# Kernel tuning notes

Measured on AMD Instinct MI355X. Metric: run time of the kernel, lower is better.

## Reference

```python
import jax, jax.numpy as jnp
import numpy as np

B, N, D_M, H, D_K, R, GRID = 2, 2048, 128, 8, 16, 4, 64


def setup_inputs() -> dict:
    key = jax.random.key(0)
    ks = jax.random.split(key, 12)
    z = jax.random.normal(ks[0], (B, N, D_M), dtype=jnp.float32)
    patch_token = jax.random.normal(ks[1], (B, 1, D_M), dtype=jnp.float32)
    positions = jax.random.randint(ks[2], (B, N, 2), 0, GRID, dtype=jnp.int32)
    alive_mask = (jax.random.uniform(ks[3], (B, N, 1)) > 0.1).astype(jnp.float32)
    s = 0.02
    Wq = jax.random.normal(ks[4], (D_M, H * D_K), dtype=jnp.float32) * s
    Wk = jax.random.normal(ks[5], (D_M, H * D_K), dtype=jnp.float32) * s
    Wv = jax.random.normal(ks[6], (D_M, H * D_K), dtype=jnp.float32) * s
    Wo = jax.random.normal(ks[7], (H * D_K, D_M), dtype=jnp.float32) * s
    bq = jnp.zeros((H * D_K,), jnp.float32)
    bk = jnp.zeros((H * D_K,), jnp.float32)
    bv = jnp.zeros((H * D_K,), jnp.float32)
    bo = jnp.zeros((D_M,), jnp.float32)
    rel_bias = jax.random.normal(ks[8], (H, 2 * R + 1, 2 * R + 1), dtype=jnp.float32) * s
    return {"z": z, "patch_token": patch_token, "positions": positions, "alive_mask": alive_mask,
            "Wq": Wq, "bq": bq, "Wk": Wk, "bk": bk, "Wv": Wv, "bv": bv, "Wo": Wo, "bo": bo,
            "rel_bias": rel_bias}


def reference(z, patch_token, positions, alive_mask, Wq, bq, Wk, bk, Wv, bv, Wo, bo, rel_bias):
    B_, N_, _ = z.shape
    H_ = rel_bias.shape[0]
    R_ = (rel_bias.shape[1] - 1) // 2
    dk = Wq.shape[1] // H_
    alive = alive_mask                                   # [B,N,1] float 0/1
    z_a = z * alive
    tokens = jnp.concatenate([z_a, patch_token], axis=1)  # [B,N+1,d_m]
    q = (z_a @ Wq + bq).reshape(B_, N_, H_, dk).transpose(0, 2, 1, 3)       # [B,H,N,dk]
    k = (tokens @ Wk + bk).reshape(B_, N_ + 1, H_, dk).transpose(0, 2, 1, 3)
    v = (tokens @ Wv + bv).reshape(B_, N_ + 1, H_, dk).transpose(0, 2, 1, 3)
    q = q * alive[:, None]                               # [B,1,N,1] broadcast
    logits = jnp.einsum('bhnd,bhmd->bhnm', q, k) / jnp.sqrt(jnp.float32(dk))  # [B,H,N,N+1]
    # Chebyshev mask (delta = pos_i - pos_j)
    delta = positions[:, :, None, :] - positions[:, None, :, :]               # [B,N,N,2]
    cheb = jnp.maximum(jnp.abs(delta[..., 0]), jnp.abs(delta[..., 1]))
    alive_j = alive[:, :, 0] > 0
    not_self = ~jnp.eye(N_, dtype=bool)
    allowed = (cheb <= R_) & alive_j[:, None, :] & not_self[None]
    mask_agents = jnp.where(allowed, 0.0, -1e9).astype(jnp.float32)           # [B,N,N]
    # Relative-position bias (torch uses delta_rel = pos_j - pos_i = -delta)
    dx = -delta[..., 0] + R_
    dy = -delta[..., 1] + R_
    valid = (dx >= 0) & (dx <= 2 * R_) & (dy >= 0) & (dy <= 2 * R_)
    flat = jnp.clip(dx, 0, 2 * R_) * (2 * R_ + 1) + jnp.clip(dy, 0, 2 * R_)   # [B,N,N] int
    table = rel_bias.reshape(H_, -1)
    rel = jnp.moveaxis(jnp.take(table, flat, axis=1), 0, 1)                   # [B,H,N,N]
    rel = rel * valid[:, None].astype(jnp.float32)
    add = mask_agents[:, None] + rel                                          # [B,H,N,N]
    logits = logits + jnp.pad(add, ((0, 0), (0, 0), (0, 0), (0, 1)))          # patch col: mask 0, no bias
    logits = jnp.where(alive[:, None] > 0, logits, -1e9)                      # dead queries
    attn = jax.nn.softmax(logits, axis=-1)
    out = jnp.einsum('bhnm,bhmd->bhnd', attn, v)
    out = out.transpose(0, 2, 1, 3).reshape(B_, N_, H_ * dk)
    out = (out @ Wo + bo) * alive
    return out
```

## Files before the change

### kernel.cpp

```cpp
#include <hip/hip_runtime.h>
#include <hip/hip_fp16.h>
#include <math.h>

#define BB 2
#define NN 2048
#define NP1 2049
#define DM 128
#define NH 8
#define DK 16
#define RWIN 4
#define GRID_W 64
#define QPB 4
#define CAND_PQ 160

__device__ __forceinline__ void unpack8(uint4 r, float* f) {
    float2 t;
    t = __half22float2(*(const __half2*)&r.x); f[0] = t.x; f[1] = t.y;
    t = __half22float2(*(const __half2*)&r.y); f[2] = t.x; f[3] = t.y;
    t = __half22float2(*(const __half2*)&r.z); f[4] = t.x; f[5] = t.y;
    t = __half22float2(*(const __half2*)&r.w); f[6] = t.x; f[7] = t.y;
}


#define QKV_ROWS 8

__global__ __launch_bounds__(384) void qkv_kernel(
    const float* __restrict__ z, const float* __restrict__ patch,
    const float* __restrict__ Wq, const float* __restrict__ bq,
    const float* __restrict__ Wk, const float* __restrict__ bk,
    const float* __restrict__ Wv, const float* __restrict__ bv,
    float* __restrict__ q, __half* __restrict__ k, __half* __restrict__ v) {
    __shared__ float zrow[QKV_ROWS][DM];
    const int tid = threadIdx.x;
    const int mat = tid >> 7;
    const int rem = tid & 127;
    const int cg = rem & 31;
    const int rs = rem >> 5;
    const int r0 = blockIdx.x * QKV_ROWS;
    const int NROWS = BB * NP1;

    if (tid < QKV_ROWS * DM / 4) {
        int r = tid >> 5, q4 = tid & 31;
        int row = r0 + r;
        float4 val = make_float4(0.f, 0.f, 0.f, 0.f);
        if (row < NROWS) {
            int b = row / NP1, ti = row % NP1;
            const float* src = (ti < NN) ? (z + ((size_t)b * NN + ti) * DM)
                                         : (patch + (size_t)b * DM);
            val = ((const float4*)src)[q4];
        }
        *((float4*)&zrow[r][q4 * 4]) = val;
    }
    __syncthreads();

    const float* W    = (mat == 0) ? Wq : (mat == 1) ? Wk : Wv;
    const float* bias = (mat == 0) ? bq : (mat == 1) ? bk : bv;

    float a0x = 0.f, a0y = 0.f, a0z = 0.f, a0w = 0.f;
    float a1x = 0.f, a1y = 0.f, a1z = 0.f, a1w = 0.f;
#pragma unroll 8
    for (int kk = 0; kk < DM; ++kk) {
        float4 w4 = *((const float4*)(W + kk * DM + cg * 4));
        float z0 = zrow[rs][kk];
        float z1 = zrow[rs + 4][kk];
        a0x = fmaf(z0, w4.x, a0x); a0y = fmaf(z0, w4.y, a0y);
        a0z = fmaf(z0, w4.z, a0z); a0w = fmaf(z0, w4.w, a0w);
        a1x = fmaf(z1, w4.x, a1x); a1y = fmaf(z1, w4.y, a1y);
        a1z = fmaf(z1, w4.z, a1z); a1w = fmaf(z1, w4.w, a1w);
    }
    float4 b4 = *((const float4*)(bias + cg * 4));
    float4 o0 = make_float4(a0x + b4.x, a0y + b4.y, a0z + b4.z, a0w + b4.w);
    float4 o1 = make_float4(a1x + b4.x, a1y + b4.y, a1z + b4.z, a1w + b4.w);

#pragma unroll
    for (int rr = 0; rr < 2; ++rr) {
        int row = r0 + rs + rr * 4;
        if (row >= NROWS) break;
        float4 val = rr ? o1 : o0;
        int b = row / NP1, ti = row % NP1;
        if (mat == 0) {
            if (ti < NN) ((float4*)(q + ((size_t)b * NN + ti) * DM))[cg] = val;
        } else {
            __half2 p0 = __floats2half2_rn(val.x, val.y);
            __half2 p1 = __floats2half2_rn(val.z, val.w);
            uint2 st;
            st.x = *(unsigned int*)&p0;
            st.y = *(unsigned int*)&p1;
            __half* dst = ((mat == 1) ? k : v) + ((size_t)b * NP1 + ti) * DM;
            ((uint2*)dst)[cg] = st;
        }
    }
}


__global__ __launch_bounds__(256) void attn_out_kernel(
    const float* __restrict__ q, const __half* __restrict__ k, const __half* __restrict__ v,
    const int* __restrict__ positions, const float* __restrict__ alive,
    const float* __restrict__ rel_bias, const float* __restrict__ Wo,
    const float* __restrict__ bo, float* __restrict__ out) {
    const int tid = threadIdx.x;
    const int qq = tid >> 6;
    const int l6 = tid & 63;
    const int h = l6 >> 3;
    const int s = l6 & 7;
    const int r0 = blockIdx.x * QPB;
    const int b = r0 >> 11;
    const int bi = r0 + qq;

    __shared__ float sbias[NH * 81];
    __shared__ int   spx[QPB], spy[QPB];
    __shared__ float sal[QPB];
    __shared__ int   mcount[QPB];
    __shared__ int   cand[QPB][CAND_PQ];
    __shared__ float po[QPB * 8][DM + 1];
    __shared__ float pl[QPB * 8][NH + 1];
    __shared__ float srow[QPB][DM + 1];

    if (tid < QPB) {
        mcount[tid] = 0;
        int gbi = r0 + tid;
        spx[tid] = positions[gbi * 2 + 0];
        spy[tid] = positions[gbi * 2 + 1];
        sal[tid] = alive[gbi];
    }
    for (int t = tid; t < NH * 81; t += 256) sbias[t] = rel_bias[t];

    const __half* kb = k + (size_t)b * NP1 * DM;
    const __half* vb = v + (size_t)b * NP1 * DM;

    float qf[16];
    {
        const float4* qr = (const float4*)(q + (size_t)bi * DM + h * DK);
#pragma unroll
        for (int e = 0; e < 4; ++e) {
            float4 t4 = qr[e];
            qf[e * 4 + 0] = t4.x * 0.25f; qf[e * 4 + 1] = t4.y * 0.25f;
            qf[e * 4 + 2] = t4.z * 0.25f; qf[e * 4 + 3] = t4.w * 0.25f;
        }
    }

    __syncthreads();

    int qx[QPB], qy[QPB], qi[QPB];
    float qa[QPB];
#pragma unroll
    for (int u = 0; u < QPB; ++u) {
        qx[u] = spx[u]; qy[u] = spy[u]; qa[u] = sal[u];
        qi[u] = (r0 + u) & (NN - 1);
    }

    {
        const int2* pb = (const int2*)(positions + (size_t)b * NN * 2);
        const float* ab = alive + (size_t)b * NN;
#pragma unroll
        for (int u = 0; u < NN / 256; ++u) {
            int j = u * 256 + tid;
            int2 pj = pb[j];
            float aj = ab[j];
            if (aj > 0.5f) {
                int packed = j | (pj.x << 16) | (pj.y << 24);
#pragma unroll
                for (int qn = 0; qn < QPB; ++qn) {
                    int dx = pj.x - qx[qn]; dx = dx < 0 ? -dx : dx;
                    int dy = pj.y - qy[qn]; dy = dy < 0 ? -dy : dy;
                    int ch = dx > dy ? dx : dy;
                    if (ch <= RWIN && j != qi[qn] && qa[qn] > 0.5f) {
                        int slot = atomicAdd(&mcount[qn], 1);
                        if (slot < CAND_PQ) cand[qn][slot] = packed;
                    }
                }
            }
        }
    }
    __syncthreads();
    int M = mcount[qq]; if (M > CAND_PQ) M = CAND_PQ;
    const int pix = qx[qq], piy = qy[qq];

    float l = 0.f;
    float o[16];
#pragma unroll
    for (int e = 0; e < 16; ++e) o[e] = 0.f;

    if (s == 0) {
        const uint4* kr = (const uint4*)(kb + (size_t)NN * DM + h * DK);
        uint4 ka = kr[0], kb4 = kr[1];
        const uint4* vr = (const uint4*)(vb + (size_t)NN * DM + h * DK);
        uint4 va = vr[0], vb4 = vr[1];
        float kf[16], vf[16];
        unpack8(ka, kf); unpack8(kb4, kf + 8);
        unpack8(va, vf); unpack8(vb4, vf + 8);
        float d = 0.f;
#pragma unroll
        for (int e = 0; e < 16; ++e) d = fmaf(qf[e], kf[e], d);
        float p = __expf(d);
        l += p;
#pragma unroll
        for (int e = 0; e < 16; ++e) o[e] = fmaf(p, vf[e], o[e]);
    }

    for (int t = s; t < M; t += 8) {
        int packed = cand[qq][t];
        int j = packed & 0xFFFF;
        const uint4* kr = (const uint4*)(kb + (size_t)j * DM + h * DK);
        uint4 ka = kr[0], kb4 = kr[1];
        const uint4* vr = (const uint4*)(vb + (size_t)j * DM + h * DK);
        uint4 va = vr[0], vb4 = vr[1];
        float kf[16], vf[16];
        unpack8(ka, kf); unpack8(kb4, kf + 8);
        unpack8(va, vf); unpack8(vb4, vf + 8);
        float d = 0.f;
#pragma unroll
        for (int e = 0; e < 16; ++e) d = fmaf(qf[e], kf[e], d);
        int pjx = (packed >> 16) & 0xFF;
        int pjy = (packed >> 24) & 0xFF;
        float bias = sbias[h * 81 + (pjx - pix + RWIN) * 9 + (pjy - piy + RWIN)];
        float p = __expf(d + bias);
        l += p;
#pragma unroll
        for (int e = 0; e < 16; ++e) o[e] = fmaf(p, vf[e], o[e]);
    }

    {
        const int prow = qq * 8 + s;
#pragma unroll
        for (int e = 0; e < 16; ++e) po[prow][h * DK + e] = o[e];
        pl[prow][h] = l;
    }
    __syncthreads();
    {
        const int c = tid & 127;
        const int g = tid >> 7;
        const int ch = c >> 4;
#pragma unroll
        for (int qn = 0; qn < 2; ++qn) {
            int qq2 = g * 2 + qn;
            float acc = 0.f, lh = 0.f;
#pragma unroll
            for (int ss = 0; ss < 8; ++ss) {
                acc += po[qq2 * 8 + ss][c];
                lh  += pl[qq2 * 8 + ss][ch];
            }
            srow[qq2][c] = acc / lh;
        }
    }
    __syncthreads();

    {
        const int oq = qq;
        const int half = l6 >> 5;
        const int m = l6 & 31;
        const float* Wb = Wo + (size_t)half * 64 * DM + m * 4;
        const float* sr = &srow[oq][half * 64];
        float ax = 0.f, ay = 0.f, az = 0.f, aw = 0.f;
#pragma unroll 16
        for (int kk = 0; kk < 64; ++kk) {
            float sv = sr[kk];
            float4 w4 = *((const float4*)(Wb + (size_t)kk * DM));
            ax = fmaf(sv, w4.x, ax); ay = fmaf(sv, w4.y, ay);
            az = fmaf(sv, w4.z, az); aw = fmaf(sv, w4.w, aw);
        }
        ax += __shfl_xor(ax, 32, 64); ay += __shfl_xor(ay, 32, 64);
        az += __shfl_xor(az, 32, 64); aw += __shfl_xor(aw, 32, 64);
        if (half == 0) {
            float ga = sal[oq] > 0.5f ? 1.f : 0.f;
            float4 b4 = *((const float4*)(bo + m * 4));
            float4 r;
            r.x = (ax + b4.x) * ga; r.y = (ay + b4.y) * ga;
            r.z = (az + b4.z) * ga; r.w = (aw + b4.w) * ga;
            ((float4*)(out + (size_t)(r0 + oq) * DM))[m] = r;
        }
    }
}

extern "C" void kernel_launch(void* const* d_in, const int* in_sizes, int n_in,
                              void* d_out, int out_size, void* d_ws, size_t ws_size,
                              hipStream_t stream) {
    const float* z         = (const float*)d_in[0];
    const float* patch     = (const float*)d_in[1];
    const int*   positions = (const int*)d_in[2];
    const float* alive     = (const float*)d_in[3];
    const float* Wq        = (const float*)d_in[4];
    const float* bq        = (const float*)d_in[5];
    const float* Wk        = (const float*)d_in[6];
    const float* bk        = (const float*)d_in[7];
    const float* Wv        = (const float*)d_in[8];
    const float* bv        = (const float*)d_in[9];
    const float* Wo        = (const float*)d_in[10];
    const float* bo        = (const float*)d_in[11];
    const float* rel_bias  = (const float*)d_in[12];
    float* out = (float*)d_out;

    char* ws = (char*)d_ws;
    size_t off = 0;
    auto alloc = [&](size_t bytes) -> void* {
        void* p = ws + off;
        off += (bytes + 255) & ~(size_t)255;
        return p;
    };
    float*  q = (float*)alloc((size_t)BB * NN * DM * 4);
    __half* k = (__half*)alloc((size_t)BB * NP1 * DM * 2);
    __half* v = (__half*)alloc((size_t)BB * NP1 * DM * 2);

    qkv_kernel<<<(BB * NP1 + QKV_ROWS - 1) / QKV_ROWS, 384, 0, stream>>>(z, patch, Wq, bq, Wk, bk, Wv, bv, q, k, v);
    attn_out_kernel<<<(BB * NN) / QPB, 256, 0, stream>>>(q, k, v, positions, alive, rel_bias, Wo, bo, out);
}
```

Baseline: 121.1 us.

## Replace LDS partial-sum reduction with wavefront shuffle reduce-scatter in attention

In the attention kernel, the eight per-slot partial outputs and softmax denominators were combined through large shared arrays, which needed an extra barrier. They are now reduced with a butterfly shuffle reduce-scatter inside the wavefront, and each lane writes its two normalized outputs straight into srow. This removes one __syncthreads and about 20KB of LDS, which may also raise occupancy. Two smaller changes ride along: the QKV projection reads z from LDS as float4 instead of scalars, and the relative-bias table is loaded with float4 copies.

```diff
diff --git a/kernel.cpp b/kernel.cpp
--- a/kernel.cpp
+++ b/kernel.cpp
@@ -58,15 +58,22 @@
 
     float a0x = 0.f, a0y = 0.f, a0z = 0.f, a0w = 0.f;
     float a1x = 0.f, a1y = 0.f, a1z = 0.f, a1w = 0.f;
-#pragma unroll 8
-    for (int kk = 0; kk < DM; ++kk) {
-        float4 w4 = *((const float4*)(W + kk * DM + cg * 4));
-        float z0 = zrow[rs][kk];
-        float z1 = zrow[rs + 4][kk];
-        a0x = fmaf(z0, w4.x, a0x); a0y = fmaf(z0, w4.y, a0y);
-        a0z = fmaf(z0, w4.z, a0z); a0w = fmaf(z0, w4.w, a0w);
-        a1x = fmaf(z1, w4.x, a1x); a1y = fmaf(z1, w4.y, a1y);
-        a1z = fmaf(z1, w4.z, a1z); a1w = fmaf(z1, w4.w, a1w);
+#pragma unroll 2
+    for (int kk4 = 0; kk4 < DM; kk4 += 4) {
+        float4 z0v = *((const float4*)&zrow[rs][kk4]);
+        float4 z1v = *((const float4*)&zrow[rs + 4][kk4]);
+        const float* zp0 = (const float*)&z0v;
+        const float* zp1 = (const float*)&z1v;
+#pragma unroll
+        for (int t = 0; t < 4; ++t) {
+            float4 w4 = *((const float4*)(W + (size_t)(kk4 + t) * DM + cg * 4));
+            float z0 = zp0[t];
+            float z1 = zp1[t];
+            a0x = fmaf(z0, w4.x, a0x); a0y = fmaf(z0, w4.y, a0y);
+            a0z = fmaf(z0, w4.z, a0z); a0w = fmaf(z0, w4.w, a0w);
+            a1x = fmaf(z1, w4.x, a1x); a1y = fmaf(z1, w4.y, a1y);
+            a1z = fmaf(z1, w4.z, a1z); a1w = fmaf(z1, w4.w, a1w);
+        }
     }
     float4 b4 = *((const float4*)(bias + cg * 4));
     float4 o0 = make_float4(a0x + b4.x, a0y + b4.y, a0z + b4.z, a0w + b4.w);
@@ -112,9 +119,7 @@
     __shared__ float sal[QPB];
     __shared__ int   mcount[QPB];
     __shared__ int   cand[QPB][CAND_PQ];
-    __shared__ float po[QPB * 8][DM + 1];
-    __shared__ float pl[QPB * 8][NH + 1];
-    __shared__ float srow[QPB][DM + 1];
+    __shared__ float srow[QPB][DM];
 
     if (tid < QPB) {
         mcount[tid] = 0;
@@ -123,7 +128,7 @@
         spy[tid] = positions[gbi * 2 + 1];
         sal[tid] = alive[gbi];
     }
-    for (int t = tid; t < NH * 81; t += 256) sbias[t] = rel_bias[t];
+    if (tid < NH * 81 / 4) ((float4*)sbias)[tid] = ((const float4*)rel_bias)[tid];
 
     const __half* kb = k + (size_t)b * NP1 * DM;
     const __half* vb = v + (size_t)b * NP1 * DM;
@@ -220,28 +225,42 @@
         for (int e = 0; e < 16; ++e) o[e] = fmaf(p, vf[e], o[e]);
     }
 
-    {
-        const int prow = qq * 8 + s;
-#pragma unroll
-        for (int e = 0; e < 16; ++e) po[prow][h * DK + e] = o[e];
-        pl[prow][h] = l;
-    }
-    __syncthreads();
-    {
-        const int c = tid & 127;
-        const int g = tid >> 7;
-        const int ch = c >> 4;
-#pragma unroll
-        for (int qn = 0; qn < 2; ++qn) {
-            int qq2 = g * 2 + qn;
-            float acc = 0.f, lh = 0.f;
-#pragma unroll
-            for (int ss = 0; ss < 8; ++ss) {
-                acc += po[qq2 * 8 + ss][c];
-                lh  += pl[qq2 * 8 + ss][ch];
-            }
-            srow[qq2][c] = acc / lh;
-        }
+    float r2_0, r2_1;
+    {
+        float r8[8];
+        const bool hi4 = (s & 4) != 0;
+#pragma unroll
+        for (int e = 0; e < 8; ++e) {
+            float a = o[e]     + __shfl_xor(o[e],     4, 64);
+            float bq_ = o[e + 8] + __shfl_xor(o[e + 8], 4, 64);
+            r8[e] = hi4 ? bq_ : a;
+        }
+        float r4[4];
+        const bool hi2 = (s & 2) != 0;
+#pragma unroll
+        for (int e = 0; e < 4; ++e) {
+            float a = r8[e]     + __shfl_xor(r8[e],     2, 64);
+            float bq_ = r8[e + 4] + __shfl_xor(r8[e + 4], 2, 64);
+            r4[e] = hi2 ? bq_ : a;
+        }
+        const bool hi1 = (s & 1) != 0;
+#pragma unroll
+        for (int e = 0; e < 2; ++e) {
+            float a = r4[e]     + __shfl_xor(r4[e],     1, 64);
+            float bq_ = r4[e + 2] + __shfl_xor(r4[e + 2], 1, 64);
+            float r = hi1 ? bq_ : a;
+            if (e == 0) r2_0 = r; else r2_1 = r;
+        }
+        l += __shfl_xor(l, 1, 64);
+        l += __shfl_xor(l, 2, 64);
+        l += __shfl_xor(l, 4, 64);
+    }
+    {
+        float linv = 1.f / l;
+        float2 st;
+        st.x = r2_0 * linv;
+        st.y = r2_1 * linv;
+        *((float2*)&srow[qq][h * DK + s * 2]) = st;
     }
     __syncthreads();
 
```

Result: no change. 121.6 us (+0.4%).
